# Performance work log

Hardware: AMD Instinct MI355X
Metric: run time of the kernel (lower is better)

Reference implementation:

```python
import jax, jax.numpy as jnp
import numpy as np


def setup_inputs() -> dict:
    key = jax.random.key(0)
    k1, k2, k3, k4 = jax.random.split(key, 4)
    B, T, C, H = 4, 4096, 1024, 64
    x = jax.random.normal(k1, (B, T, C), dtype=jnp.float32)
    Wq = jax.random.normal(k2, (C, H), dtype=jnp.float32) * (C ** -0.5)
    Wk = jax.random.normal(k3, (C, H), dtype=jnp.float32) * (C ** -0.5)
    Wv = jax.random.normal(k4, (C, H), dtype=jnp.float32) * (C ** -0.5)
    return {"x": x, "Wq": Wq, "Wk": Wk, "Wv": Wv}


def reference(x, Wq, Wk, Wv):
    B, T, C = x.shape
    q = jnp.einsum('btc,ch->bth', x, Wq)  # [B,T,H]
    k = jnp.einsum('btc,ch->bth', x, Wk)
    v = jnp.einsum('btc,ch->bth', x, Wv)
    # NOTE: original scales by C**0.5 (embed_dim), not head_size**0.5
    scale = jnp.asarray(C, x.dtype) ** 0.5
    wei = jnp.einsum('bth,bsh->bts', q, k) / scale  # [B,T,T]
    causal = jnp.tril(jnp.ones((T, T), dtype=bool))
    wei = jnp.where(causal, wei, -jnp.inf)
    wei = jax.nn.softmax(wei, axis=-1)  # dropout p=0.0 -> identity
    return jnp.einsum('bts,bsh->bth', wei, v)  # [B,T,H]
```

## Files before the change

kernel.cpp:

```cpp
#include <hip/hip_runtime.h>
#include <hip/hip_bf16.h>

typedef __bf16 bf16;
typedef __bf16 bf16x8 __attribute__((ext_vector_type(8)));
typedef __bf16 bf16x4 __attribute__((ext_vector_type(4)));
typedef float  f32x4  __attribute__((ext_vector_type(4)));

#define MFMA16(A, B, C) __builtin_amdgcn_mfma_f32_16x16x32_bf16((A), (B), (C), 0, 0, 0)

static constexpr int Bn = 4;
static constexpr int T  = 4096;
static constexpr int Cd = 1024;
static constexpr int H  = 64;
static constexpr int NG = 192;
static constexpr int CH = 8;
static constexpr int SLOTS_PER_B = 288;
static constexpr float QSCALE = 0.045084220f;

__device__ inline void dma16(const void* g, void* l) {
    __builtin_amdgcn_global_load_lds(
        (const __attribute__((address_space(1))) unsigned int*)g,
        (__attribute__((address_space(3))) unsigned int*)l, 16, 0, 0);
}

__device__ inline bf16x8 cvt_bf16x8(float4 a, float4 b) {
    bf16x8 r;
    r[0] = (bf16)a.x; r[1] = (bf16)a.y; r[2] = (bf16)a.z; r[3] = (bf16)a.w;
    r[4] = (bf16)b.x; r[5] = (bf16)b.y; r[6] = (bf16)b.z; r[7] = (bf16)b.w;
    return r;
}

__global__ __launch_bounds__(256) void wt_kernel(const float* __restrict__ Wq,
                                                 const float* __restrict__ Wk,
                                                 const float* __restrict__ Wv,
                                                 bf16* __restrict__ Wt) {
    __shared__ float s[64][65];
    const int cb = blockIdx.x;
    const int m  = blockIdx.y;
    const float* W = (m == 0) ? Wq : (m == 1) ? Wk : Wv;
    for (int i = threadIdx.x; i < 64 * 64; i += 256) {
        const int c = i >> 6, h = i & 63;
        s[c][h] = W[(cb * 64 + c) * H + h];
    }
    __syncthreads();
    for (int i = threadIdx.x; i < 64 * 64; i += 256) {
        const int n = i >> 6, c = i & 63;
        Wt[(m * 64 + n) * Cd + cb * 64 + c] = (bf16)s[c][n];
    }
}

__global__ __launch_bounds__(512, 4) void proj_kernel(const float* __restrict__ x,
                                                      const bf16* __restrict__ Wt,
                                                      bf16* __restrict__ qw,
                                                      bf16* __restrict__ kw,
                                                      bf16* __restrict__ vtw) {
    const int tid  = threadIdx.x;
    const int lane = tid & 63;
    const int w    = tid >> 6;
    const int wr   = w >> 2;
    const int wc   = w & 3;
    const int ml   = lane & 15;
    const int quad = lane >> 4;

    const long r0 = (long)blockIdx.x * 32;

    __shared__ float sX[2][32][64];
    __shared__ bf16  sW[2][192][64];

    const int xrow = w * 4 + (lane >> 4);
    const float* gx = x + (r0 + xrow) * Cd + (((lane & 15) ^ (xrow & 15)) << 2);
    const int wchunk = ((lane & 7) ^ (lane >> 3)) << 3;
    const bf16* gw0 = Wt + (long)(w * 24 + 0 + (lane >> 3)) * Cd + wchunk;
    const bf16* gw1 = Wt + (long)(w * 24 + 8 + (lane >> 3)) * Cd + wchunk;
    const bf16* gw2 = Wt + (long)(w * 24 + 16 + (lane >> 3)) * Cd + wchunk;

    f32x4 acc[3];
    #pragma unroll
    for (int j = 0; j < 3; ++j) acc[j] = f32x4{0.f, 0.f, 0.f, 0.f};

    dma16(gx, &sX[0][w * 4][0]);
    dma16(gw0, &sW[0][w * 24 + 0][0]);
    dma16(gw1, &sW[0][w * 24 + 8][0]);
    dma16(gw2, &sW[0][w * 24 + 16][0]);

    const int arow = wr * 16 + ml;
    const int brow0 = wc * 48 + ml;
    const int bsw = ml & 7;

    int buf = 0;
    for (int kb = 0; kb < Cd; kb += 64) {
        const bool pre = (kb + 64 < Cd);
        if (pre) {
            dma16(gx + kb + 64, &sX[buf ^ 1][w * 4][0]);
            dma16(gw0 + kb + 64, &sW[buf ^ 1][w * 24 + 0][0]);
            dma16(gw1 + kb + 64, &sW[buf ^ 1][w * 24 + 8][0]);
            dma16(gw2 + kb + 64, &sW[buf ^ 1][w * 24 + 16][0]);
            asm volatile("s_waitcnt vmcnt(4)" ::: "memory");
        } else {
            asm volatile("s_waitcnt vmcnt(0)" ::: "memory");
        }
        __builtin_amdgcn_sched_barrier(0);
        __builtin_amdgcn_s_barrier();
        __builtin_amdgcn_sched_barrier(0);

        #pragma unroll
        for (int ks = 0; ks < 2; ++ks) {
            const int ca = (ks * 8 + quad * 2) ^ ml;
            const float4 lo = *(const float4*)&sX[buf][arow][ca << 2];
            const float4 hi = *(const float4*)&sX[buf][arow][(ca ^ 1) << 2];
            const bf16x8 af = cvt_bf16x8(lo, hi);
            const int cb0 = (ks * 4 + quad) ^ bsw;
            acc[0] = MFMA16(af, *(const bf16x8*)&sW[buf][brow0 + 0][cb0 << 3], acc[0]);
            acc[1] = MFMA16(af, *(const bf16x8*)&sW[buf][brow0 + 16][cb0 << 3], acc[1]);
            acc[2] = MFMA16(af, *(const bf16x8*)&sW[buf][brow0 + 32][cb0 << 3], acc[2]);
        }

        if (pre) {
            __builtin_amdgcn_sched_barrier(0);
            __builtin_amdgcn_s_barrier();
        }
        buf ^= 1;
    }

    const int b = (int)(r0 >> 12);
    const long rowb = r0 + wr * 16 + quad * 4;
    const int  tloc = (int)(rowb & 4095);

    #pragma unroll
    for (int f = 0; f < 3; ++f) {
        const int base = wc * 48 + f * 16;
        const int sel  = base >> 6;
        const int h    = (base & 63) + ml;
        if (sel == 0) {
            #pragma unroll
            for (int rr = 0; rr < 4; ++rr)
                qw[(rowb + rr) * H + h] = (bf16)(acc[f][rr] * QSCALE);
        } else if (sel == 1) {
            #pragma unroll
            for (int rr = 0; rr < 4; ++rr)
                kw[(rowb + rr) * H + h] = (bf16)acc[f][rr];
        } else {
            bf16x4 pv;
            #pragma unroll
            for (int rr = 0; rr < 4; ++rr) pv[rr] = (bf16)acc[f][rr];
            *(bf16x4*)(vtw + ((long)(b * H + h)) * T + tloc) = pv;
        }
    }
}

__global__ __launch_bounds__(256, 4) void attn_kernel(const bf16* __restrict__ qw,
                                                      const bf16* __restrict__ kw,
                                                      const bf16* __restrict__ vtw,
                                                      float* __restrict__ pO,
                                                      float* __restrict__ pL) {
    const int u = blockIdx.x;
    int g = 0;
    #pragma unroll
    for (int gg = 1; gg < 8; ++gg) if (u >= (gg * (gg + 1)) / 2) g = gg;
    const int c  = u - (g * (g + 1)) / 2;
    const int r  = blockIdx.y;
    const int b  = blockIdx.z;
    const int qt = g * 8 + r;

    const int tid  = threadIdx.x;
    const int lane = tid & 63;
    const int w    = tid >> 6;
    const int ml   = lane & 15;
    const int quad = lane >> 4;
    const int mx   = ml & 7;

    __shared__ bf16 sK[2][64][64];
    __shared__ bf16 sVt[2][64][64];
    __shared__ bf16 sP[4][16][64];

    const int t0 = qt * 64;

    const bf16* q0 = qw + ((long)b * T + t0 + w * 16 + ml) * H;
    const bf16x8 aq0 = *(const bf16x8*)(q0 + quad * 8);
    const bf16x8 aq1 = *(const bf16x8*)(q0 + 32 + quad * 8);

    f32x4 O[4];
    #pragma unroll
    for (int ht = 0; ht < 4; ++ht) O[ht] = f32x4{0.f, 0.f, 0.f, 0.f};
    float lrow[4] = {0.f, 0.f, 0.f, 0.f};

    const int trow = t0 + w * 16 + quad * 4;
    const int jt0 = c * CH;
    const int jt1 = (c == g) ? qt + 1 : (c + 1) * CH;

    const int drow = w * 8 + (lane >> 3);
    const int dsw  = ((lane & 7) ^ (drow & 7)) << 3;
    const bf16* kbase = kw + (long)b * T * H;
    const bf16* vbase = vtw + (long)b * H * T;
    const long koffA = (long)drow * H + dsw;
    const long koffB = koffA + 32 * H;
    const long voffA = (long)drow * T + dsw;
    const long voffB = voffA + (long)32 * T;

    {
        const long ks0 = (long)jt0 * 64;
        dma16(kbase + ks0 * H + koffA, &sK[0][w * 8][0]);
        dma16(kbase + ks0 * H + koffB, &sK[0][32 + w * 8][0]);
        dma16(vbase + ks0 + voffA, &sVt[0][w * 8][0]);
        dma16(vbase + ks0 + voffB, &sVt[0][32 + w * 8][0]);
    }

    int buf = 0;
    for (int jt = jt0; jt < jt1; ++jt) {
        const bool pre = (jt + 1 < jt1);
        if (pre) {
            const long ksn = (long)(jt + 1) * 64;
            dma16(kbase + ksn * H + koffA, &sK[buf ^ 1][w * 8][0]);
            dma16(kbase + ksn * H + koffB, &sK[buf ^ 1][32 + w * 8][0]);
            dma16(vbase + ksn + voffA, &sVt[buf ^ 1][w * 8][0]);
            dma16(vbase + ksn + voffB, &sVt[buf ^ 1][32 + w * 8][0]);
            asm volatile("s_waitcnt vmcnt(4)" ::: "memory");
        } else {
            asm volatile("s_waitcnt vmcnt(0)" ::: "memory");
        }
        __builtin_amdgcn_sched_barrier(0);
        __builtin_amdgcn_s_barrier();
        __builtin_amdgcn_sched_barrier(0);

        const int s0 = jt * 64;
        const bool diag = (jt == qt);
        #pragma unroll
        for (int nt = 0; nt < 4; ++nt) {
            f32x4 sacc = f32x4{0.f, 0.f, 0.f, 0.f};
            sacc = MFMA16(aq0, *(const bf16x8*)&sK[buf][nt * 16 + ml][(quad ^ mx) << 3], sacc);
            sacc = MFMA16(aq1, *(const bf16x8*)&sK[buf][nt * 16 + ml][((4 + quad) ^ mx) << 3], sacc);
            const int col = s0 + nt * 16 + ml;
            #pragma unroll
            for (int rr = 0; rr < 4; ++rr) {
                const float p = (diag && col > trow + rr) ? 0.f : exp2f(sacc[rr]);
                lrow[rr] += p;
                const int row = quad * 4 + rr;
                const int sw  = (row & 7) ^ ((row & 8) >> 2);
                sP[w][row][(((nt * 2 + (ml >> 3)) ^ sw) << 3) | (ml & 7)] = (bf16)p;
            }
        }
        asm volatile("s_waitcnt lgkmcnt(0)" ::: "memory");
        __builtin_amdgcn_sched_barrier(0);

        #pragma unroll
        for (int ks = 0; ks < 2; ++ks) {
            const int pch = ((ks * 4 + quad) ^ (ml & 7) ^ ((ml & 8) >> 2)) << 3;
            const bf16x8 ap = *(const bf16x8*)&sP[w][ml][pch];
            #pragma unroll
            for (int ht = 0; ht < 4; ++ht)
                O[ht] = MFMA16(ap,
                    *(const bf16x8*)&sVt[buf][ht * 16 + ml][(((ks << 2) + quad) ^ mx) << 3],
                    O[ht]);
        }

        if (pre) {
            __builtin_amdgcn_sched_barrier(0);
            __builtin_amdgcn_s_barrier();
        }
        buf ^= 1;
    }

    #pragma unroll
    for (int d = 1; d < 16; d <<= 1)
        #pragma unroll
        for (int rr = 0; rr < 4; ++rr)
            lrow[rr] += __shfl_xor(lrow[rr], d, 64);

    const long slot = (long)b * SLOTS_PER_B + (long)(g + 1) * (4 * g + r) + c;
    float* po = pO + slot * 4096 + (w * 16) * 64;
    #pragma unroll
    for (int ht = 0; ht < 4; ++ht)
        #pragma unroll
        for (int rr = 0; rr < 4; ++rr)
            po[(quad * 4 + rr) * 64 + ht * 16 + ml] = O[ht][rr];
    if (ml == 0) {
        #pragma unroll
        for (int rr = 0; rr < 4; ++rr)
            pL[slot * 64 + w * 16 + quad * 4 + rr] = lrow[rr];
    }
}

__global__ __launch_bounds__(256) void combine_kernel(const float* __restrict__ pO,
                                                      const float* __restrict__ pL,
                                                      float* __restrict__ out) {
    const int qt = blockIdx.x;
    const int b  = blockIdx.y;
    const int g  = qt >> 3, r = qt & 7;
    const int nch = g + 1;
    const long slot0 = (long)b * SLOTS_PER_B + (long)(g + 1) * (4 * g + r);

    const int tid = threadIdx.x;
    const int row = tid >> 2;
    const int q4  = tid & 3;

    f32x4 o[4];
    #pragma unroll
    for (int j = 0; j < 4; ++j) o[j] = f32x4{0.f, 0.f, 0.f, 0.f};
    float l = 0.f;

    for (int cc = 0; cc < nch; ++cc) {
        const float* po = pO + (slot0 + cc) * 4096 + row * 64 + q4 * 16;
        #pragma unroll
        for (int j = 0; j < 4; ++j) o[j] += *(const f32x4*)(po + j * 4);
        l += pL[(slot0 + cc) * 64 + row];
    }
    const float inv = 1.f / l;
    float* op = out + ((long)b * T + qt * 64 + row) * H + q4 * 16;
    #pragma unroll
    for (int j = 0; j < 4; ++j) {
        f32x4 v = o[j];
        v[0] *= inv; v[1] *= inv; v[2] *= inv; v[3] *= inv;
        *(f32x4*)(op + j * 4) = v;
    }
}

extern "C" void kernel_launch(void* const* d_in, const int* in_sizes, int n_in,
                              void* d_out, int out_size, void* d_ws, size_t ws_size,
                              hipStream_t stream) {
    const float* x  = (const float*)d_in[0];
    const float* Wq = (const float*)d_in[1];
    const float* Wk = (const float*)d_in[2];
    const float* Wv = (const float*)d_in[3];
    float* out = (float*)d_out;

    char* ws = (char*)d_ws;
    const size_t WT_BYTES = (size_t)NG * Cd * sizeof(bf16);
    const size_t QK_BYTES = (size_t)Bn * T * H * sizeof(bf16);
    const size_t PO_OFF   = WT_BYTES + 3 * QK_BYTES;
    const size_t PO_BYTES = (size_t)Bn * SLOTS_PER_B * 4096 * sizeof(float);
    bf16*  Wt  = (bf16*)ws;
    bf16*  qw  = (bf16*)(ws + WT_BYTES);
    bf16*  kw  = (bf16*)(ws + WT_BYTES + QK_BYTES);
    bf16*  vtw = (bf16*)(ws + WT_BYTES + 2 * QK_BYTES);
    float* pO  = (float*)(ws + PO_OFF);
    float* pL  = (float*)(ws + PO_OFF + PO_BYTES);

    wt_kernel<<<dim3(16, 3), dim3(256), 0, stream>>>(Wq, Wk, Wv, Wt);
    proj_kernel<<<dim3((Bn * T) / 32), dim3(512), 0, stream>>>(x, Wt, qw, kw, vtw);
    attn_kernel<<<dim3(36, CH, Bn), dim3(256), 0, stream>>>(qw, kw, vtw, pO, pL);
    combine_kernel<<<dim3(T / 64, Bn), dim3(256), 0, stream>>>(pO, pL, out);
}
```

Baseline: 152.3 us.

## Deepen projection x prefetch pipeline, use single barrier per step, add MFMA priority

The projection kernel now keeps a 4-deep ring of x tiles (prefetch distance 3) and a 2-deep ring of W tiles, issues the next loads after a single barrier per k-step, and fully unrolls the 16-step loop with explicit vmcnt waits. The attention kernel also drops to one barrier per KV tile, waiting for all outstanding loads before issuing the next prefetch. Both kernels raise wave priority around MFMA sections. The aim is to hide global-load latency and cut barrier count, at the cost of more LDS per block and a shallower effective prefetch in attention.

Result: no change. 151.8 us (median of 2 runs) (-0.3%).

```diff
diff --git a/kernel.cpp b/kernel.cpp
--- a/kernel.cpp
+++ b/kernel.cpp
@@ -21,6 +21,12 @@
     __builtin_amdgcn_global_load_lds(
         (const __attribute__((address_space(1))) unsigned int*)g,
         (__attribute__((address_space(3))) unsigned int*)l, 16, 0, 0);
+}
+
+__device__ __forceinline__ void waitcnt_vm(int n) {
+    if (n == 0)      asm volatile("s_waitcnt vmcnt(0)" ::: "memory");
+    else if (n == 1) asm volatile("s_waitcnt vmcnt(1)" ::: "memory");
+    else             asm volatile("s_waitcnt vmcnt(2)" ::: "memory");
 }
 
 __device__ inline bf16x8 cvt_bf16x8(float4 a, float4 b) {
@@ -64,7 +70,7 @@
 
     const long r0 = (long)blockIdx.x * 32;
 
-    __shared__ float sX[2][32][64];
+    __shared__ float sX[4][32][64];
     __shared__ bf16  sW[2][192][64];
 
     const int xrow = w * 4 + (lane >> 4);
@@ -82,44 +88,41 @@
     dma16(gw0, &sW[0][w * 24 + 0][0]);
     dma16(gw1, &sW[0][w * 24 + 8][0]);
     dma16(gw2, &sW[0][w * 24 + 16][0]);
+    dma16(gx + 64,  &sX[1][w * 4][0]);
+    dma16(gx + 128, &sX[2][w * 4][0]);
 
     const int arow = wr * 16 + ml;
     const int brow0 = wc * 48 + ml;
     const int bsw = ml & 7;
 
-    int buf = 0;
-    for (int kb = 0; kb < Cd; kb += 64) {
-        const bool pre = (kb + 64 < Cd);
-        if (pre) {
-            dma16(gx + kb + 64, &sX[buf ^ 1][w * 4][0]);
-            dma16(gw0 + kb + 64, &sW[buf ^ 1][w * 24 + 0][0]);
-            dma16(gw1 + kb + 64, &sW[buf ^ 1][w * 24 + 8][0]);
-            dma16(gw2 + kb + 64, &sW[buf ^ 1][w * 24 + 16][0]);
-            asm volatile("s_waitcnt vmcnt(4)" ::: "memory");
-        } else {
-            asm volatile("s_waitcnt vmcnt(0)" ::: "memory");
-        }
+    #pragma unroll
+    for (int t = 0; t < 16; ++t) {
+        waitcnt_vm(t == 0 ? 2 : (t <= 13 ? 1 : 0));
         __builtin_amdgcn_sched_barrier(0);
         __builtin_amdgcn_s_barrier();
         __builtin_amdgcn_sched_barrier(0);
 
+        if (t + 1 < 16) {
+            dma16(gw0 + (t + 1) * 64, &sW[(t + 1) & 1][w * 24 + 0][0]);
+            dma16(gw1 + (t + 1) * 64, &sW[(t + 1) & 1][w * 24 + 8][0]);
+            dma16(gw2 + (t + 1) * 64, &sW[(t + 1) & 1][w * 24 + 16][0]);
+        }
+        if (t + 3 < 16) dma16(gx + (t + 3) * 64, &sX[(t + 3) & 3][w * 4][0]);
+
+        const int bx = t & 3, bw = t & 1;
+        __builtin_amdgcn_s_setprio(1);
         #pragma unroll
         for (int ks = 0; ks < 2; ++ks) {
             const int ca = (ks * 8 + quad * 2) ^ ml;
-            const float4 lo = *(const float4*)&sX[buf][arow][ca << 2];
-            const float4 hi = *(const float4*)&sX[buf][arow][(ca ^ 1) << 2];
+            const float4 lo = *(const float4*)&sX[bx][arow][ca << 2];
+            const float4 hi = *(const float4*)&sX[bx][arow][(ca ^ 1) << 2];
             const bf16x8 af = cvt_bf16x8(lo, hi);
             const int cb0 = (ks * 4 + quad) ^ bsw;
-            acc[0] = MFMA16(af, *(const bf16x8*)&sW[buf][brow0 + 0][cb0 << 3], acc[0]);
-            acc[1] = MFMA16(af, *(const bf16x8*)&sW[buf][brow0 + 16][cb0 << 3], acc[1]);
-            acc[2] = MFMA16(af, *(const bf16x8*)&sW[buf][brow0 + 32][cb0 << 3], acc[2]);
-        }
-
-        if (pre) {
-            __builtin_amdgcn_sched_barrier(0);
-            __builtin_amdgcn_s_barrier();
-        }
-        buf ^= 1;
+            acc[0] = MFMA16(af, *(const bf16x8*)&sW[bw][brow0 + 0][cb0 << 3], acc[0]);
+            acc[1] = MFMA16(af, *(const bf16x8*)&sW[bw][brow0 + 16][cb0 << 3], acc[1]);
+            acc[2] = MFMA16(af, *(const bf16x8*)&sW[bw][brow0 + 32][cb0 << 3], acc[2]);
+        }
+        __builtin_amdgcn_s_setprio(0);
     }
 
     const int b = (int)(r0 >> 12);
@@ -207,28 +210,28 @@
 
     int buf = 0;
     for (int jt = jt0; jt < jt1; ++jt) {
-        const bool pre = (jt + 1 < jt1);
-        if (pre) {
+        asm volatile("s_waitcnt vmcnt(0)" ::: "memory");
+        __builtin_amdgcn_sched_barrier(0);
+        __builtin_amdgcn_s_barrier();
+        __builtin_amdgcn_sched_barrier(0);
+
+        if (jt + 1 < jt1) {
             const long ksn = (long)(jt + 1) * 64;
             dma16(kbase + ksn * H + koffA, &sK[buf ^ 1][w * 8][0]);
             dma16(kbase + ksn * H + koffB, &sK[buf ^ 1][32 + w * 8][0]);
             dma16(vbase + ksn + voffA, &sVt[buf ^ 1][w * 8][0]);
             dma16(vbase + ksn + voffB, &sVt[buf ^ 1][32 + w * 8][0]);
-            asm volatile("s_waitcnt vmcnt(4)" ::: "memory");
-        } else {
-            asm volatile("s_waitcnt vmcnt(0)" ::: "memory");
-        }
-        __builtin_amdgcn_sched_barrier(0);
-        __builtin_amdgcn_s_barrier();
-        __builtin_amdgcn_sched_barrier(0);
+        }
 
         const int s0 = jt * 64;
         const bool diag = (jt == qt);
         #pragma unroll
         for (int nt = 0; nt < 4; ++nt) {
             f32x4 sacc = f32x4{0.f, 0.f, 0.f, 0.f};
+            __builtin_amdgcn_s_setprio(1);
             sacc = MFMA16(aq0, *(const bf16x8*)&sK[buf][nt * 16 + ml][(quad ^ mx) << 3], sacc);
             sacc = MFMA16(aq1, *(const bf16x8*)&sK[buf][nt * 16 + ml][((4 + quad) ^ mx) << 3], sacc);
+            __builtin_amdgcn_s_setprio(0);
             const int col = s0 + nt * 16 + ml;
             #pragma unroll
             for (int rr = 0; rr < 4; ++rr) {
@@ -242,6 +245,7 @@
         asm volatile("s_waitcnt lgkmcnt(0)" ::: "memory");
         __builtin_amdgcn_sched_barrier(0);
 
+        __builtin_amdgcn_s_setprio(1);
         #pragma unroll
         for (int ks = 0; ks < 2; ++ks) {
             const int pch = ((ks * 4 + quad) ^ (ml & 7) ^ ((ml & 8) >> 2)) << 3;
@@ -252,11 +256,8 @@
                     *(const bf16x8*)&sVt[buf][ht * 16 + ml][(((ks << 2) + quad) ^ mx) << 3],
                     O[ht]);
         }
-
-        if (pre) {
-            __builtin_amdgcn_sched_barrier(0);
-            __builtin_amdgcn_s_barrier();
-        }
+        __builtin_amdgcn_s_setprio(0);
+
         buf ^= 1;
     }
 
```
